# Performance work log

Measured on AMD Instinct MI355X. Metric: run time of the kernel, lower is better.

## Reference

```python
import jax, jax.numpy as jnp
import numpy as np

# PyTorch LSTM gate order: i, f, g, o. Dropout layers are identity in eval mode.

def _lstm_step(w_ih, w_hh, b):
    def step(carry, xt):
        h, c = carry
        g = xt @ w_ih.T + h @ w_hh.T + b
        i, f, gg, o = jnp.split(g, 4, axis=-1)
        c = jax.nn.sigmoid(f) * c + jax.nn.sigmoid(i) * jnp.tanh(gg)
        h = jax.nn.sigmoid(o) * jnp.tanh(c)
        return (h, c), h
    return step


def bilstm(x, wf_ih, wf_hh, bf_ih, bf_hh, wb_ih, wb_hh, bb_ih, bb_hh):
    # x: [B, T, D] -> out: [B, T, 2H]
    B = x.shape[0]
    H = wf_hh.shape[1]
    xt = jnp.swapaxes(x, 0, 1)  # [T, B, D]
    init = (jnp.zeros((B, H), x.dtype), jnp.zeros((B, H), x.dtype))
    _, hf = jax.lax.scan(_lstm_step(wf_ih, wf_hh, bf_ih + bf_hh), init, xt)
    _, hb = jax.lax.scan(_lstm_step(wb_ih, wb_hh, bb_ih + bb_hh), init, xt[::-1])
    hb = hb[::-1]
    return jnp.swapaxes(jnp.concatenate([hf, hb], axis=-1), 0, 1)


def setup_inputs() -> dict:
    key = jax.random.key(0)
    ks = iter(jax.random.split(key, 64))
    d = {"x": jax.random.normal(next(ks), (1024, 1024, 8), jnp.float32)}
    layer_dims = [(16, 20), (40, 20), (40, 10), (20, 10)]
    for li, (din, H) in enumerate(layer_dims, start=1):
        for dr in ("f", "b"):
            d[f"w{li}{dr}_ih"] = 0.1 * jax.random.normal(next(ks), (4 * H, din), jnp.float32)
            d[f"w{li}{dr}_hh"] = 0.1 * jax.random.normal(next(ks), (4 * H, H), jnp.float32)
            d[f"b{li}{dr}_ih"] = 0.1 * jax.random.normal(next(ks), (4 * H,), jnp.float32)
            d[f"b{li}{dr}_hh"] = 0.1 * jax.random.normal(next(ks), (4 * H,), jnp.float32)
    d["fc_w"] = 0.1 * jax.random.normal(next(ks), (1, 20), jnp.float32)
    d["fc_b"] = 0.1 * jax.random.normal(next(ks), (1,), jnp.float32)
    return d


def reference(x,
              w1f_ih, w1f_hh, b1f_ih, b1f_hh, w1b_ih, w1b_hh, b1b_ih, b1b_hh,
              w2f_ih, w2f_hh, b2f_ih, b2f_hh, w2b_ih, w2b_hh, b2b_ih, b2b_hh,
              w3f_ih, w3f_hh, b3f_ih, b3f_hh, w3b_ih, w3b_hh, b3b_ih, b3b_hh,
              w4f_ih, w4f_hh, b4f_ih, b4f_hh, w4b_ih, w4b_hh, b4b_ih, b4b_hh,
              fc_w, fc_b):
    # lag-1 concat: [B,T,8] -> [B,T,16]
    x_lag = jnp.concatenate([jnp.zeros_like(x[:, :1, :]), x[:, :-1, :]], axis=1)
    h = jnp.concatenate([x, x_lag], axis=2)
    h = bilstm(h, w1f_ih, w1f_hh, b1f_ih, b1f_hh, w1b_ih, w1b_hh, b1b_ih, b1b_hh)
    h = bilstm(h, w2f_ih, w2f_hh, b2f_ih, b2f_hh, w2b_ih, w2b_hh, b2b_ih, b2b_hh)
    h = bilstm(h, w3f_ih, w3f_hh, b3f_ih, b3f_hh, w3b_ih, w3b_hh, b3b_ih, b3b_hh)
    h = bilstm(h, w4f_ih, w4f_hh, b4f_ih, b4f_hh, w4b_ih, w4b_hh, b4b_ih, b4b_hh)
    h = h[:, -1, :]  # [B, 20]
    return jax.nn.sigmoid(h @ fc_w.T + fc_b)
```

## Files before the change

### kernel.cpp

```cpp
#include <hip/hip_runtime.h>
#include <hip/hip_fp16.h>
#include <stdint.h>

#define B_TOTAL 1024
#define T_TOTAL 1024
#define LOG2E 1.44269504088896f

typedef _Float16 f16x2 __attribute__((ext_vector_type(2)));

__device__ __forceinline__ float dot2w(uint32_t xw, uint32_t ww, float acc) {
#if __has_builtin(__builtin_amdgcn_fdot2)
    return __builtin_amdgcn_fdot2(__builtin_bit_cast(f16x2, xw),
                                  __builtin_bit_cast(f16x2, ww), acc, false);
#else
    f16x2 xv = __builtin_bit_cast(f16x2, xw);
    f16x2 wv = __builtin_bit_cast(f16x2, ww);
    return acc + (float)xv.x * (float)wv.x + (float)xv.y * (float)wv.y;
#endif
}

__device__ __forceinline__ uint32_t packf2(float a, float b) {
    f16x2 t;
    t.x = (_Float16)a;
    t.y = (_Float16)b;
    return __builtin_bit_cast(uint32_t, t);
}

__device__ __forceinline__ float sigm_(float z) {
    float e = __builtin_amdgcn_exp2f(-LOG2E * z);
    return __builtin_amdgcn_rcpf(1.0f + e);
}
__device__ __forceinline__ float tanh_(float z) {
    float e = __builtin_amdgcn_exp2f((2.0f * LOG2E) * z);
    float r = __builtin_amdgcn_rcpf(1.0f + e);
    return __builtin_fmaf(-2.0f, r, 1.0f);
}

__device__ __forceinline__ void wavebar() {
#if __has_builtin(__builtin_amdgcn_wave_barrier)
    __builtin_amdgcn_wave_barrier();
#endif
}

template <int DIN, int H, bool LAYER1, bool STORE_ALL>
__global__ void __launch_bounds__(64)
__attribute__((amdgpu_waves_per_eu(1, 1))) lstm_scan(
    const float* __restrict__ x,
    const __half* __restrict__ inbuf,
    const float* __restrict__ wihf, const float* __restrict__ whhf,
    const float* __restrict__ bihf, const float* __restrict__ bhhf,
    const float* __restrict__ wihb, const float* __restrict__ whhb,
    const float* __restrict__ bihb, const float* __restrict__ bhhb,
    __half* __restrict__ outbuf,
    float* __restrict__ lasth)
{
    constexpr int GPW    = 64 / H;
    constexpr int ND     = DIN / 2;
    constexpr int NH     = H / 2;
    constexpr int HS_DW  = (H == 20) ? 12 : 8;
    constexpr int CHUNK  = (GPW == 3) ? 16 : 8;
    constexpr int NCHUNK = T_TOTAL / CHUNK;
    constexpr int NDX    = LAYER1 ? 4 : ND;
    constexpr int XROWS  = LAYER1 ? (CHUNK + 1) : CHUNK;
    constexpr int XWORDS = XROWS * GPW * NDX;
    constexpr int NLOAD  = (XWORDS + 63) / 64;

    const int dir  = blockIdx.y;
    const int lane = threadIdx.x;
    const int g    = lane / H;
    const int j    = lane - g * H;
    const int b    = blockIdx.x * GPW + g;
    const bool valid = (g < GPW) && (b < B_TOTAL);
    const int bs   = valid ? b : (B_TOTAL - 1);

    const float* w_ih = dir ? wihb : wihf;
    const float* w_hh = dir ? whhb : whhf;
    const float* b_ih = dir ? bihb : bihf;
    const float* b_hh = dir ? bhhb : bhhf;

    __shared__ uint32_t xsm[2 * XWORDS];
    __shared__ uint32_t hsm[GPW + 1][HS_DW];

    uint32_t wih2[4][ND];
    uint32_t whh2[4][NH];
    float bias[4];
#pragma unroll
    for (int q = 0; q < 4; ++q) {
        const int r = q * H + j;
#pragma unroll
        for (int d = 0; d < ND; ++d)
            wih2[q][d] = packf2(w_ih[r * DIN + 2 * d], w_ih[r * DIN + 2 * d + 1]);
#pragma unroll
        for (int k = 0; k < NH; ++k)
            whh2[q][k] = packf2(w_hh[r * H + 2 * k], w_hh[r * H + 2 * k + 1]);
        bias[q] = b_ih[r] + b_hh[r];
    }
#pragma unroll
    for (int q = 0; q < 4; ++q) {
#pragma unroll
        for (int d = 0; d < ND; ++d) asm volatile("" : "+v"(wih2[q][d]));
#pragma unroll
        for (int k = 0; k < NH; ++k) asm volatile("" : "+v"(whh2[q][k]));
        asm volatile("" : "+v"(bias[q]));
    }

    uint32_t greg[NLOAD];

    auto stage_load = [&](int c) {
        const int sbase = c * CHUNK;
#pragma unroll
        for (int i = 0; i < NLOAD; ++i) {
            const int idx = lane + 64 * i;
            uint32_t v = 0;
            if (idx < XWORDS) {
                const int row = idx / (GPW * NDX);
                const int rem = idx - row * (GPW * NDX);
                const int r   = rem / NDX;
                const int d   = rem - r * NDX;
                const int br  = blockIdx.x * GPW + r;
                int t;
                if constexpr (LAYER1)
                    t = dir ? (T_TOTAL - 1 - sbase) - row : (sbase - 1) + row;
                else
                    t = dir ? (T_TOTAL - 1) - (sbase + row) : sbase + row;
                if (t >= 0 && t < T_TOTAL && br < B_TOTAL) {
                    if constexpr (LAYER1) {
                        const float2 p = ((const float2*)(x + (size_t)br * (T_TOTAL * 8) +
                                                          (size_t)t * 8))[d];
                        v = packf2(p.x, p.y);
                    } else {
                        v = ((const uint32_t*)inbuf)[(size_t)t * (B_TOTAL * ND) +
                                                     (size_t)br * ND + d];
                    }
                }
            }
            greg[i] = v;
        }
    };
    auto stage_write = [&](int buf) {
#pragma unroll
        for (int i = 0; i < NLOAD; ++i) {
            const int idx = lane + 64 * i;
            if (idx < XWORDS) xsm[buf * XWORDS + idx] = greg[i];
        }
    };

    auto xread = [&](int buf, int row, uint32_t* dst) {
        const uint32_t* p = &xsm[buf * XWORDS + row * (GPW * NDX) + g * NDX];
        if constexpr (NDX % 4 == 0) {
#pragma unroll
            for (int d = 0; d < NDX; d += 4) {
                uint4 v = *(const uint4*)(p + d);
                dst[d] = v.x; dst[d + 1] = v.y; dst[d + 2] = v.z; dst[d + 3] = v.w;
            }
        } else {
#pragma unroll
            for (int d = 0; d < NDX; d += 2) {
                uint2 v = *(const uint2*)(p + d);
                dst[d] = v.x; dst[d + 1] = v.y;
            }
        }
    };

    const int tstep = dir ? -1 : 1;
    int tt = dir ? (T_TOTAL - 1) : 0;

    __half* op = nullptr;
    ptrdiff_t opstep = 0;
    if constexpr (STORE_ALL) {
        op = outbuf + (size_t)tt * (B_TOTAL * 2 * H) + (size_t)bs * (2 * H) + dir * H + j;
        opstep = (ptrdiff_t)tstep * (B_TOTAL * 2 * H);
    }

    float c_st = 0.0f;
    float hlast = 0.0f;
    ((__half*)&hsm[g][0])[j] = __float2half(0.0f);
    wavebar();

    stage_load(0);
    stage_write(0);

    auto tail = [&](const uint32_t* hd, float a0, float a1, float a2, float a3) {
#pragma unroll
        for (int k = 0; k < NH; ++k) {
            a0 = dot2w(hd[k], whh2[0][k], a0);
            a1 = dot2w(hd[k], whh2[1][k], a1);
            a2 = dot2w(hd[k], whh2[2][k], a2);
            a3 = dot2w(hd[k], whh2[3][k], a3);
        }
        const float iv = sigm_(a0);
        const float fv = sigm_(a1);
        const float gv = tanh_(a2);
        const float ov = sigm_(a3);
        c_st = __builtin_fmaf(fv, c_st, iv * gv);
        const float h = ov * tanh_(c_st);
        ((__half*)&hsm[g][0])[j] = __float2half(h);
        wavebar();
        if constexpr (STORE_ALL) {
            if (valid) *op = __float2half(h);
            op += opstep;
        } else {
            hlast = h;
        }
        tt += tstep;
    };

    if constexpr (LAYER1) {
        uint32_t cur4[4], lag4[4], nrow[4];
        xread(0, dir ? 0 : 1, cur4);
        xread(0, dir ? 1 : 0, lag4);

        int buf = 0;
        for (int c = 0; c < NCHUNK; ++c) {
#pragma unroll
            for (int k = 0; k < CHUNK; ++k) {
                uint32_t hd[NH];
#pragma unroll
                for (int q = 0; q < NH; ++q) hd[q] = hsm[g][q];

                if (k == 0 && c + 1 < NCHUNK) stage_load(c + 1);

                float a0 = bias[0], a1 = bias[1], a2 = bias[2], a3 = bias[3];
#pragma unroll
                for (int d = 0; d < 4; ++d) {
                    a0 = dot2w(cur4[d], wih2[0][d], a0);
                    a1 = dot2w(cur4[d], wih2[1][d], a1);
                    a2 = dot2w(cur4[d], wih2[2][d], a2);
                    a3 = dot2w(cur4[d], wih2[3][d], a3);
                }
#pragma unroll
                for (int d = 0; d < 4; ++d) {
                    a0 = dot2w(lag4[d], wih2[0][4 + d], a0);
                    a1 = dot2w(lag4[d], wih2[1][4 + d], a1);
                    a2 = dot2w(lag4[d], wih2[2][4 + d], a2);
                    a3 = dot2w(lag4[d], wih2[3][4 + d], a3);
                }

                if (k < CHUNK - 1) xread(buf, k + 2, nrow);
                else               xread(buf ^ 1, 1, nrow);

                if (k == CHUNK / 2 && c + 1 < NCHUNK) stage_write(buf ^ 1);

                tail(hd, a0, a1, a2, a3);

                if (dir == 0) {
#pragma unroll
                    for (int d = 0; d < 4; ++d) { lag4[d] = cur4[d]; cur4[d] = nrow[d]; }
                } else {
#pragma unroll
                    for (int d = 0; d < 4; ++d) { cur4[d] = lag4[d]; lag4[d] = nrow[d]; }
                }
            }
            buf ^= 1;
        }
    } else {
        uint32_t xcA[ND], xcB[ND];
        xread(0, 0, xcA);

        int buf = 0;
        for (int c = 0; c < NCHUNK; ++c) {
#pragma unroll
            for (int k = 0; k < CHUNK; ++k) {
                const uint32_t* xc = (k & 1) ? xcB : xcA;
                uint32_t*       xn = (k & 1) ? xcA : xcB;

                uint32_t hd[NH];
#pragma unroll
                for (int q = 0; q < NH; ++q) hd[q] = hsm[g][q];

                if (k == 0 && c + 1 < NCHUNK) stage_load(c + 1);

                float a0 = bias[0], a1 = bias[1], a2 = bias[2], a3 = bias[3];
#pragma unroll
                for (int d = 0; d < ND; ++d) {
                    a0 = dot2w(xc[d], wih2[0][d], a0);
                    a1 = dot2w(xc[d], wih2[1][d], a1);
                    a2 = dot2w(xc[d], wih2[2][d], a2);
                    a3 = dot2w(xc[d], wih2[3][d], a3);
                }

                if (k < CHUNK - 1) xread(buf, k + 1, xn);
                else               xread(buf ^ 1, 0, xn);

                if (k == CHUNK / 2 && c + 1 < NCHUNK) stage_write(buf ^ 1);

                tail(hd, a0, a1, a2, a3);
            }
            buf ^= 1;
        }
    }

    if constexpr (!STORE_ALL) {
        if (valid) lasth[b * H + j] = hlast;
    }
}

__global__ void final_kernel(const __half* __restrict__ l3out,
                             const float* __restrict__ hf4,
                             const float* __restrict__ w_ih,
                             const float* __restrict__ b_ih,
                             const float* __restrict__ b_hh,
                             const float* __restrict__ fc_w,
                             const float* __restrict__ fc_b,
                             float* __restrict__ out)
{
    const int b = blockIdx.x * blockDim.x + threadIdx.x;
    if (b >= B_TOTAL) return;

    float in4[20];
    const __half* p = l3out + (size_t)(T_TOTAL - 1) * (B_TOTAL * 20) + (size_t)b * 20;
#pragma unroll
    for (int i = 0; i < 20; ++i) in4[i] = __half2float(p[i]);

    float z = fc_b[0];
#pragma unroll
    for (int k = 0; k < 10; ++k) z += fc_w[k] * hf4[b * 10 + k];

#pragma unroll
    for (int k = 0; k < 10; ++k) {
        float gi = b_ih[k]      + b_hh[k];
        float gg = b_ih[20 + k] + b_hh[20 + k];
        float go = b_ih[30 + k] + b_hh[30 + k];
#pragma unroll
        for (int i = 0; i < 20; ++i) {
            const float xi = in4[i];
            gi += w_ih[k * 20 + i]        * xi;
            gg += w_ih[(20 + k) * 20 + i] * xi;
            go += w_ih[(30 + k) * 20 + i] * xi;
        }
        const float cc = sigm_(gi) * tanh_(gg);
        const float hb = sigm_(go) * tanh_(cc);
        z += fc_w[10 + k] * hb;
    }
    out[b] = sigm_(z);
}

extern "C" void kernel_launch(void* const* d_in, const int* in_sizes, int n_in,
                              void* d_out, int out_size, void* d_ws, size_t ws_size,
                              hipStream_t stream) {
    const float* x = (const float*)d_in[0];
    auto W = [&](int li, int dr, int k) -> const float* {
        return (const float*)d_in[1 + (li - 1) * 8 + dr * 4 + k];
    };
    const float* fc_w = (const float*)d_in[33];
    const float* fc_b = (const float*)d_in[34];
    float* out = (float*)d_out;

    __half* buf0 = (__half*)d_ws;
    __half* buf1 = buf0 + (size_t)T_TOTAL * B_TOTAL * 40;
    float* hf4 = (float*)(buf1 + (size_t)T_TOTAL * B_TOTAL * 40);

    lstm_scan<16, 20, true, true><<<dim3(342, 2, 1), 64, 0, stream>>>(
        x, nullptr,
        W(1,0,0), W(1,0,1), W(1,0,2), W(1,0,3),
        W(1,1,0), W(1,1,1), W(1,1,2), W(1,1,3),
        buf0, nullptr);

    lstm_scan<40, 20, false, true><<<dim3(342, 2, 1), 64, 0, stream>>>(
        nullptr, buf0,
        W(2,0,0), W(2,0,1), W(2,0,2), W(2,0,3),
        W(2,1,0), W(2,1,1), W(2,1,2), W(2,1,3),
        buf1, nullptr);

    lstm_scan<40, 10, false, true><<<dim3(171, 2, 1), 64, 0, stream>>>(
        nullptr, buf1,
        W(3,0,0), W(3,0,1), W(3,0,2), W(3,0,3),
        W(3,1,0), W(3,1,1), W(3,1,2), W(3,1,3),
        buf0, nullptr);

    lstm_scan<20, 10, false, false><<<dim3(171, 1, 1), 64, 0, stream>>>(
        nullptr, buf0,
        W(4,0,0), W(4,0,1), W(4,0,2), W(4,0,3),
        W(4,0,0), W(4,0,1), W(4,0,2), W(4,0,3),
        nullptr, hf4);

    final_kernel<<<dim3(4, 1, 1), 256, 0, stream>>>(
        buf0, hf4, W(4,1,0), W(4,1,2), W(4,1,3), fc_w, fc_b, out);
}
```

Measured before the change: 1.665 ms.

## Hoist input projections out of recurrent LSTM scans into parallel GEMM kernels

Adds a parallel projection kernel that computes x·W_ih for every timestep and both directions ahead of time, storing gate pre-activations in fp16. A new scan kernel then only performs the recurrent h·W_hh dot products, reading the precomputed gates through a four-deep register prefetch. This takes the input-projection work off the serial critical path of each timestep. The cost is extra global-memory traffic for the large gate buffers and more kernel launches. The old fused path is kept as a fallback when the workspace is too small.

Result: no change. 1.656 ms (-0.6%).

```diff
diff --git a/kernel.cpp b/kernel.cpp
--- a/kernel.cpp
+++ b/kernel.cpp
@@ -42,9 +42,232 @@
 #endif
 }
 
+template <int DIN, int H, int NDIR, bool L1X>
+__global__ void __launch_bounds__(256) proj_kernel(
+    const float* __restrict__ x,
+    const __half* __restrict__ inbuf,
+    const float* __restrict__ w0,
+    const float* __restrict__ w1,
+    __half* __restrict__ g0,
+    __half* __restrict__ g1)
+{
+    constexpr int NDW   = DIN / 2;
+    constexpr int O4H   = 4 * H;
+    constexpr int OUT   = NDIR * O4H;
+    constexpr int RPB   = 16;
+    constexpr int TPR   = 16;
+    constexpr int OPT   = (OUT + TPR - 1) / TPR;
+    constexpr int TILES = 8;
+    constexpr int DWR   = O4H / 2;
+
+    __shared__ uint32_t wt[NDW][OUT];
+    __shared__ uint32_t xin[RPB * NDW];
+    __shared__ uint32_t osm[RPB][OUT / 2];
+
+    const int tid = threadIdx.x;
+
+    for (int idx = tid; idx < NDW * OUT; idx += 256) {
+        const int d  = idx / OUT;
+        const int o  = idx - d * OUT;
+        const int dr = o / O4H;
+        const int oo = o - dr * O4H;
+        const int jj = oo >> 2;
+        const int qq = oo & 3;
+        const float* w = dr ? w1 : w0;
+        const int row = qq * H + jj;
+        wt[d][o] = packf2(w[row * DIN + 2 * d], w[row * DIN + 2 * d + 1]);
+    }
+
+    const int rr = tid >> 4;
+    const int li = tid & 15;
+
+    for (int tile = 0; tile < TILES; ++tile) {
+        const int r0 = (blockIdx.x * TILES + tile) * RPB;
+        __syncthreads();
+
+        if constexpr (L1X) {
+            for (int idx = tid; idx < RPB * NDW; idx += 256) {
+                const int r  = r0 + idx / NDW;
+                const int d  = idx % NDW;
+                const int bb = r >> 10;
+                const int t  = r & (T_TOTAL - 1);
+                float2 v = {0.f, 0.f};
+                if (d < 4) {
+                    v = ((const float2*)(x + ((size_t)bb * T_TOTAL + t) * 8))[d];
+                } else if (t > 0) {
+                    v = ((const float2*)(x + ((size_t)bb * T_TOTAL + t - 1) * 8))[d - 4];
+                }
+                xin[idx] = packf2(v.x, v.y);
+            }
+        } else {
+            const uint32_t* src = (const uint32_t*)inbuf + (size_t)r0 * NDW;
+            for (int idx = tid; idx < RPB * NDW; idx += 256)
+                xin[idx] = src[idx];
+        }
+        __syncthreads();
+
+        float acc[OPT];
+#pragma unroll
+        for (int oi = 0; oi < OPT; ++oi) acc[oi] = 0.f;
+#pragma unroll
+        for (int d = 0; d < NDW; ++d) {
+            const uint32_t xv = xin[rr * NDW + d];
+#pragma unroll
+            for (int oi = 0; oi < OPT; ++oi) {
+                const int o = li * OPT + oi;
+                if (OUT % TPR == 0 || o < OUT)
+                    acc[oi] = dot2w(xv, wt[d][o], acc[oi]);
+            }
+        }
+        {
+            __half* oh = (__half*)&osm[rr][0];
+#pragma unroll
+            for (int oi = 0; oi < OPT; ++oi) {
+                const int o = li * OPT + oi;
+                if (OUT % TPR == 0 || o < OUT) oh[o] = __float2half(acc[oi]);
+            }
+        }
+        __syncthreads();
+
+        for (int idx = tid; idx < RPB * (OUT / 2); idx += 256) {
+            const int r   = idx / (OUT / 2);
+            const int od  = idx - r * (OUT / 2);
+            const int dr  = od / DWR;
+            const int odd = od - dr * DWR;
+            uint32_t* dst = (uint32_t*)(dr ? g1 : g0);
+            dst[(size_t)(r0 + r) * DWR + odd] = osm[r][od];
+        }
+    }
+}
+
+template <int H, bool XMAJOR, bool STORE_ALL>
+__global__ void __launch_bounds__(64)
+__attribute__((amdgpu_waves_per_eu(1, 1))) lstm_scan2(
+    const __half* __restrict__ gxf, const __half* __restrict__ gxb,
+    const float* __restrict__ whhf, const float* __restrict__ bihf,
+    const float* __restrict__ bhhf,
+    const float* __restrict__ whhb, const float* __restrict__ bihb,
+    const float* __restrict__ bhhb,
+    __half* __restrict__ outbuf,
+    float* __restrict__ lasth)
+{
+    constexpr int GPW   = 64 / H;
+    constexpr int NH    = H / 2;
+    constexpr int HS_DW = (H == 20) ? 12 : 8;
+    constexpr int PF    = 4;
+
+    const int dir  = blockIdx.y;
+    const int lane = threadIdx.x;
+    const int g    = lane / H;
+    const int j    = lane - g * H;
+    const int b    = blockIdx.x * GPW + g;
+    const bool valid = (g < GPW) && (b < B_TOTAL);
+    const int bs   = valid ? b : (B_TOTAL - 1);
+
+    const __half* gx  = dir ? gxb : gxf;
+    const float* w_hh = dir ? whhb : whhf;
+    const float* b_i  = dir ? bihb : bihf;
+    const float* b_h  = dir ? bhhb : bhhf;
+
+    __shared__ uint32_t hsm[GPW + 1][HS_DW];
+
+    uint32_t whh2[4][NH];
+    float bias[4];
+#pragma unroll
+    for (int q = 0; q < 4; ++q) {
+        const int r = q * H + j;
+#pragma unroll
+        for (int k = 0; k < NH; ++k)
+            whh2[q][k] = packf2(w_hh[r * H + 2 * k], w_hh[r * H + 2 * k + 1]);
+        bias[q] = b_i[r] + b_h[r];
+    }
+#pragma unroll
+    for (int q = 0; q < 4; ++q) {
+#pragma unroll
+        for (int k = 0; k < NH; ++k) asm volatile("" : "+v"(whh2[q][k]));
+        asm volatile("" : "+v"(bias[q]));
+    }
+
+    const int sgn = dir ? -1 : 1;
+    const int t0  = dir ? (T_TOTAL - 1) : 0;
+    const uint32_t PSTRIDE = XMAJOR ? (uint32_t)(8 * H)
+                                    : (uint32_t)(B_TOTAL * 8 * H);
+    const uint32_t jboff = (XMAJOR ? (uint32_t)bs * T_TOTAL * 8 * H
+                                   : (uint32_t)bs * 8 * H) + (uint32_t)j * 8;
+    const char* gxc = (const char*)gx;
+
+    __half* op = nullptr;
+    ptrdiff_t opstep = 0;
+    if constexpr (STORE_ALL) {
+        op = outbuf + (size_t)t0 * (B_TOTAL * 2 * H) + (size_t)bs * (2 * H) + dir * H + j;
+        opstep = (ptrdiff_t)sgn * (B_TOTAL * 2 * H);
+    }
+
+    ((__half*)&hsm[g][0])[j] = __float2half(0.0f);
+    wavebar();
+    uint32_t hd[NH];
+#pragma unroll
+    for (int k = 0; k < NH; ++k) hd[k] = hsm[g][k];
+
+    uint2 pf[PF];
+#pragma unroll
+    for (int i = 0; i < PF; ++i) {
+        const int tp = t0 + sgn * i;
+        pf[i] = *(const uint2*)(gxc + jboff + (uint32_t)tp * PSTRIDE);
+    }
+
+    float c_st = 0.0f, hlast = 0.0f;
+
+#define STEP(I)                                                               \
+    {                                                                         \
+        const uint2 gxv = pf[I];                                              \
+        int tp = t0 + sgn * (sb + (I) + PF);                                  \
+        tp = tp < 0 ? 0 : (tp > T_TOTAL - 1 ? T_TOTAL - 1 : tp);              \
+        pf[I] = *(const uint2*)(gxc + jboff + (uint32_t)tp * PSTRIDE);        \
+        const f16x2 p01 = __builtin_bit_cast(f16x2, gxv.x);                   \
+        const f16x2 p23 = __builtin_bit_cast(f16x2, gxv.y);                   \
+        float a0 = (float)p01.x + bias[0];                                    \
+        float a1 = (float)p01.y + bias[1];                                    \
+        float a2 = (float)p23.x + bias[2];                                    \
+        float a3 = (float)p23.y + bias[3];                                    \
+        _Pragma("unroll")                                                     \
+        for (int k = 0; k < NH; ++k) {                                        \
+            a0 = dot2w(hd[k], whh2[0][k], a0);                                \
+            a1 = dot2w(hd[k], whh2[1][k], a1);                                \
+            a2 = dot2w(hd[k], whh2[2][k], a2);                                \
+            a3 = dot2w(hd[k], whh2[3][k], a3);                                \
+        }                                                                     \
+        const float iv = sigm_(a0);                                           \
+        const float fv = sigm_(a1);                                           \
+        const float gv = tanh_(a2);                                           \
+        const float ov = sigm_(a3);                                           \
+        c_st = __builtin_fmaf(fv, c_st, iv * gv);                             \
+        const float h = ov * tanh_(c_st);                                     \
+        ((__half*)&hsm[g][0])[j] = __float2half(h);                           \
+        wavebar();                                                            \
+        _Pragma("unroll")                                                     \
+        for (int k = 0; k < NH; ++k) hd[k] = hsm[g][k];                       \
+        if constexpr (STORE_ALL) {                                            \
+            if (valid) *op = __float2half(h);                                 \
+            op += opstep;                                                     \
+        } else {                                                              \
+            hlast = h;                                                        \
+        }                                                                     \
+    }
+
+    for (int sb = 0; sb < T_TOTAL; sb += PF) {
+        STEP(0) STEP(1) STEP(2) STEP(3)
+    }
+#undef STEP
+
+    if constexpr (!STORE_ALL) {
+        if (valid) lasth[b * H + j] = hlast;
+    }
+}
+
 template <int DIN, int H, bool LAYER1, bool STORE_ALL>
 __global__ void __launch_bounds__(64)
-__attribute__((amdgpu_waves_per_eu(1, 1))) lstm_scan(
+__attribute__((amdgpu_waves_per_eu(1, 1))) lstm_scan_fused(
     const float* __restrict__ x,
     const __half* __restrict__ inbuf,
     const float* __restrict__ wihf, const float* __restrict__ whhf,
@@ -144,7 +367,6 @@
             if (idx < XWORDS) xsm[buf * XWORDS + idx] = greg[i];
         }
     };
-
     auto xread = [&](int buf, int row, uint32_t* dst) {
         const uint32_t* p = &xsm[buf * XWORDS + row * (GPW * NDX) + g * NDX];
         if constexpr (NDX % 4 == 0) {
@@ -346,34 +568,71 @@
     const float* fc_b = (const float*)d_in[34];
     float* out = (float*)d_out;
 
-    __half* buf0 = (__half*)d_ws;
-    __half* buf1 = buf0 + (size_t)T_TOTAL * B_TOTAL * 40;
-    float* hf4 = (float*)(buf1 + (size_t)T_TOTAL * B_TOTAL * 40);
-
-    lstm_scan<16, 20, true, true><<<dim3(342, 2, 1), 64, 0, stream>>>(
-        x, nullptr,
-        W(1,0,0), W(1,0,1), W(1,0,2), W(1,0,3),
-        W(1,1,0), W(1,1,1), W(1,1,2), W(1,1,3),
-        buf0, nullptr);
-
-    lstm_scan<40, 20, false, true><<<dim3(342, 2, 1), 64, 0, stream>>>(
-        nullptr, buf0,
-        W(2,0,0), W(2,0,1), W(2,0,2), W(2,0,3),
-        W(2,1,0), W(2,1,1), W(2,1,2), W(2,1,3),
-        buf1, nullptr);
-
-    lstm_scan<40, 10, false, true><<<dim3(171, 2, 1), 64, 0, stream>>>(
-        nullptr, buf1,
-        W(3,0,0), W(3,0,1), W(3,0,2), W(3,0,3),
-        W(3,1,0), W(3,1,1), W(3,1,2), W(3,1,3),
-        buf0, nullptr);
-
-    lstm_scan<20, 10, false, false><<<dim3(171, 1, 1), 64, 0, stream>>>(
-        nullptr, buf0,
-        W(4,0,0), W(4,0,1), W(4,0,2), W(4,0,3),
-        W(4,0,0), W(4,0,1), W(4,0,2), W(4,0,3),
-        nullptr, hf4);
-
-    final_kernel<<<dim3(4, 1, 1), 256, 0, stream>>>(
-        buf0, hf4, W(4,1,0), W(4,1,2), W(4,1,3), fc_w, fc_b, out);
-}
+    const size_t ROWS = (size_t)T_TOTAL * B_TOTAL;
+    const size_t GXH  = ROWS * 80;
+    const size_t HH   = ROWS * 40;
+    const size_t need = (2 * GXH + 2 * HH) * sizeof(__half) +
+                        (size_t)B_TOTAL * 10 * sizeof(float);
+
+    if (ws_size >= need) {
+        __half* gxf = (__half*)d_ws;
+        __half* gxb = gxf + GXH;
+        __half* hA  = gxb + GXH;
+        __half* hB  = hA + HH;
+        float*  hf4 = (float*)(hB + HH);
+
+        proj_kernel<16, 20, 2, true><<<dim3(8192), 256, 0, stream>>>(
+            x, nullptr, W(1,0,0), W(1,1,0), gxf, gxb);
+        lstm_scan2<20, true, true><<<dim3(342, 2), 64, 0, stream>>>(
+            gxf, gxb, W(1,0,1), W(1,0,2), W(1,0,3),
+                      W(1,1,1), W(1,1,2), W(1,1,3), hA, nullptr);
+
+        proj_kernel<40, 20, 2, false><<<dim3(8192), 256, 0, stream>>>(
+            nullptr, hA, W(2,0,0), W(2,1,0), gxf, gxb);
+        lstm_scan2<20, false, true><<<dim3(342, 2), 64, 0, stream>>>(
+            gxf, gxb, W(2,0,1), W(2,0,2), W(2,0,3),
+                      W(2,1,1), W(2,1,2), W(2,1,3), hB, nullptr);
+
+        proj_kernel<40, 10, 2, false><<<dim3(8192), 256, 0, stream>>>(
+            nullptr, hB, W(3,0,0), W(3,1,0), gxf, gxb);
+        lstm_scan2<10, false, true><<<dim3(171, 2), 64, 0, stream>>>(
+            gxf, gxb, W(3,0,1), W(3,0,2), W(3,0,3),
+                      W(3,1,1), W(3,1,2), W(3,1,3), hA, nullptr);
+
+        proj_kernel<20, 10, 1, false><<<dim3(8192), 256, 0, stream>>>(
+            nullptr, hA, W(4,0,0), W(4,0,0), gxf, gxf);
+        lstm_scan2<10, false, false><<<dim3(171, 1), 64, 0, stream>>>(
+            gxf, gxf, W(4,0,1), W(4,0,2), W(4,0,3),
+                      W(4,0,1), W(4,0,2), W(4,0,3), nullptr, hf4);
+
+        final_kernel<<<dim3(4), 256, 0, stream>>>(
+            hA, hf4, W(4,1,0), W(4,1,2), W(4,1,3), fc_w, fc_b, out);
+    } else {
+        __half* buf0 = (__half*)d_ws;
+        __half* buf1 = buf0 + (size_t)T_TOTAL * B_TOTAL * 40;
+        float*  hf4  = (float*)(buf1 + (size_t)T_TOTAL * B_TOTAL * 40);
+
+        lstm_scan_fused<16, 20, true, true><<<dim3(342, 2, 1), 64, 0, stream>>>(
+            x, nullptr,
+            W(1,0,0), W(1,0,1), W(1,0,2), W(1,0,3),
+            W(1,1,0), W(1,1,1), W(1,1,2), W(1,1,3),
+            buf0, nullptr);
+        lstm_scan_fused<40, 20, false, true><<<dim3(342, 2, 1), 64, 0, stream>>>(
+            nullptr, buf0,
+            W(2,0,0), W(2,0,1), W(2,0,2), W(2,0,3),
+            W(2,1,0), W(2,1,1), W(2,1,2), W(2,1,3),
+            buf1, nullptr);
+        lstm_scan_fused<40, 10, false, true><<<dim3(171, 2, 1), 64, 0, stream>>>(
+            nullptr, buf1,
+            W(3,0,0), W(3,0,1), W(3,0,2), W(3,0,3),
+            W(3,1,0), W(3,1,1), W(3,1,2), W(3,1,3),
+            buf0, nullptr);
+        lstm_scan_fused<20, 10, false, false><<<dim3(171, 1, 1), 64, 0, stream>>>(
+            nullptr, buf0,
+            W(4,0,0), W(4,0,1), W(4,0,2), W(4,0,3),
+            W(4,0,0), W(4,0,1), W(4,0,2), W(4,0,3),
+            nullptr, hf4);
+        final_kernel<<<dim3(4, 1, 1), 256, 0, stream>>>(
+            buf0, hf4, W(4,1,0), W(4,1,2), W(4,1,3), fc_w, fc_b, out);
+    }
+}
```
